# Optimization experiments

Hardware: AMD Instinct MI355X
Metric: run time of the kernel (lower is better)

## Reference

```python
import jax, jax.numpy as jnp
import numpy as np

B, S, H, NH, HD, L, I, M = 2, 2048, 768, 12, 64, 6, 3072, 256
VOCAB, TYPES = 30522, 2
EPS = 1e-6  # layernorm epsilon and FAVOR+ numerical stabilizer


def layer_norm(x, g, b):
    mu = jnp.mean(x, axis=-1, keepdims=True)
    var = jnp.mean(jax.lax.square(x), axis=-1, keepdims=True) - jax.lax.square(mu)
    return (x - mu) * jax.lax.rsqrt(var + EPS) * g + b


def favor_attention(q, k, v, mask, proj):
    # q,k,v: [B,S,NH,HD]; proj: [M,HD] random features; mask: [B,S] float
    dn = 1.0 / np.sqrt(np.sqrt(HD))      # data normalizer for softmax kernel
    ratio = 1.0 / np.sqrt(M)
    qn, kn = q * dn, k * dn
    qp = jnp.einsum('bsnd,md->bsnm', qn, proj)
    kp = jnp.einsum('bsnd,md->bsnm', kn, proj)
    qd = 0.5 * jnp.sum(qn * qn, axis=-1, keepdims=True)
    kd = 0.5 * jnp.sum(kn * kn, axis=-1, keepdims=True)
    # stabilizers: per-position max for queries, global (seq+feature) max for keys
    q_prime = ratio * (jnp.exp(qp - qd - jnp.max(qp, axis=-1, keepdims=True)) + EPS)
    k_prime = ratio * (jnp.exp(kp - kd - jnp.max(kp, axis=(1, 3), keepdims=True)) + EPS)
    k_prime = k_prime * mask[:, :, None, None]
    kv = jnp.einsum('bsnm,bsnd->bnmd', k_prime, v)          # [B,NH,M,HD]
    num = jnp.einsum('bsnm,bnmd->bsnd', q_prime, kv)        # [B,S,NH,HD]
    den = jnp.einsum('bsnm,bnm->bsn', q_prime, jnp.sum(k_prime, axis=1))
    return num / den[..., None]


def setup_inputs() -> dict:
    key = jax.random.key(0)
    ks = jax.random.split(key, 32)
    f = lambda i, shape, s=0.02: (jax.random.normal(ks[i], shape, jnp.float32) * s)
    inp = {
        'input_ids': jax.random.randint(ks[0], (B, S), 0, VOCAB, jnp.int32),
        'token_type_ids': jax.random.randint(ks[1], (B, S), 0, TYPES, jnp.int32),
        'position_ids': jnp.tile(jnp.arange(S, dtype=jnp.int32)[None, :], (B, 1)),
        'attention_mask': jnp.ones((B, S), jnp.int32),
        'word_emb': f(2, (VOCAB, H), 0.1),
        'pos_emb': f(3, (S, H), 0.1),
        'type_emb': f(4, (TYPES, H), 0.1),
        'emb_ln_g': jnp.ones((H,), jnp.float32),
        'emb_ln_b': jnp.zeros((H,), jnp.float32),
        'wq': f(5, (L, H, NH, HD)), 'bq': jnp.zeros((L, NH, HD), jnp.float32),
        'wk': f(6, (L, H, NH, HD)), 'bk': jnp.zeros((L, NH, HD), jnp.float32),
        'wv': f(7, (L, H, NH, HD)), 'bv': jnp.zeros((L, NH, HD), jnp.float32),
        'wo': f(8, (L, NH, HD, H)), 'bo': jnp.zeros((L, H), jnp.float32),
        'ln1_g': jnp.ones((L, H), jnp.float32), 'ln1_b': jnp.zeros((L, H), jnp.float32),
        'wi': f(9, (L, H, I)), 'bi': jnp.zeros((L, I), jnp.float32),
        'wo2': f(10, (L, I, H)), 'bo2': jnp.zeros((L, H), jnp.float32),
        'ln2_g': jnp.ones((L, H), jnp.float32), 'ln2_b': jnp.zeros((L, H), jnp.float32),
        'proj': jax.random.normal(ks[11], (L, M, HD), jnp.float32),
    }
    return inp


def reference(input_ids, token_type_ids, position_ids, attention_mask,
              word_emb, pos_emb, type_emb, emb_ln_g, emb_ln_b,
              wq, bq, wk, bk, wv, bv, wo, bo, ln1_g, ln1_b,
              wi, bi, wo2, bo2, ln2_g, ln2_b, proj):
    mask = attention_mask.astype(jnp.float32)
    x = word_emb[input_ids] + pos_emb[position_ids] + type_emb[token_type_ids]
    x = layer_norm(x, emb_ln_g, emb_ln_b)
    for l in range(L):
        q = jnp.einsum('bsh,hnd->bsnd', x, wq[l]) + bq[l]
        k = jnp.einsum('bsh,hnd->bsnd', x, wk[l]) + bk[l]
        v = jnp.einsum('bsh,hnd->bsnd', x, wv[l]) + bv[l]
        att = favor_attention(q, k, v, mask, proj[l])
        att = jnp.einsum('bsnd,ndh->bsh', att, wo[l]) + bo[l]
        a = layer_norm(att + x, ln1_g[l], ln1_b[l])
        inter = jax.nn.gelu(jnp.einsum('bsh,hi->bsi', a, wi[l]) + bi[l])
        out = jnp.einsum('bsi,ih->bsh', inter, wo2[l]) + bo2[l]
        x = layer_norm(out + a, ln2_g[l], ln2_b[l])
    return x
```

## Files before the change

### kernel.cpp

```cpp
#include <hip/hip_runtime.h>
#include <hip/hip_bf16.h>

#define B_ 2
#define S_ 2048
#define H_ 768
#define NH_ 12
#define HD_ 64
#define L_ 6
#define I_ 3072
#define M_ 256
#define BS_ 4096
#define R_ 49152
#define EPS_ 1e-6f
#define DN_ 0.35355339059327373f
#define RATIO_ 0.0625f

typedef __attribute__((ext_vector_type(8))) short bf16x8;
typedef __attribute__((ext_vector_type(4))) float f32x4;

__device__ __forceinline__ void gload16(const void* g, void* l) {
    __builtin_amdgcn_global_load_lds(
        (const __attribute__((address_space(1))) void*)g,
        (__attribute__((address_space(3))) void*)l, 16, 0, 0);
}

__device__ __forceinline__ float gelu_f(float x) {
    const float c = 0.7978845608028654f;
    float x3 = x * x * x;
    return 0.5f * x * (1.0f + tanhf(c * (x + 0.044715f * x3)));
}

__device__ __forceinline__ void blockReduceSum2(float& a, float& b) {
    __shared__ float sa[4], sb[4];
    int lane = threadIdx.x & 63, wid = threadIdx.x >> 6;
    #pragma unroll
    for (int off = 32; off; off >>= 1) {
        a += __shfl_down(a, off, 64);
        b += __shfl_down(b, off, 64);
    }
    __syncthreads();
    if (lane == 0) { sa[wid] = a; sb[wid] = b; }
    __syncthreads();
    a = sa[0] + sa[1] + sa[2] + sa[3];
    b = sb[0] + sb[1] + sb[2] + sb[3];
    __syncthreads();
}

__device__ __forceinline__ float blockReduceMax(float v) {
    __shared__ float sm[4];
    int lane = threadIdx.x & 63, wid = threadIdx.x >> 6;
    #pragma unroll
    for (int off = 32; off; off >>= 1) v = fmaxf(v, __shfl_down(v, off, 64));
    __syncthreads();
    if (lane == 0) sm[wid] = v;
    __syncthreads();
    float r = fmaxf(fmaxf(sm[0], sm[1]), fmaxf(sm[2], sm[3]));
    __syncthreads();
    return r;
}

__device__ __forceinline__ float blockReduceSum(float v) {
    __shared__ float sm[4];
    int lane = threadIdx.x & 63, wid = threadIdx.x >> 6;
    #pragma unroll
    for (int off = 32; off; off >>= 1) v += __shfl_down(v, off, 64);
    __syncthreads();
    if (lane == 0) sm[wid] = v;
    __syncthreads();
    float r = sm[0] + sm[1] + sm[2] + sm[3];
    __syncthreads();
    return r;
}

template<int ACT, int OUTMODE, int RMAXOUT>
__global__ __launch_bounds__(256) void gemm_mfma_kernel(
    const __hip_bfloat16* __restrict__ A, const __hip_bfloat16* __restrict__ BT,
    const float* __restrict__ bias, void* __restrict__ Cv,
    int N, int K, int lda, int ldb, int ldc, float alpha,
    float* __restrict__ rmaxp)
{
    __shared__ __align__(16) unsigned short As[2][128][32];
    __shared__ __align__(16) unsigned short Bs[2][128][32];
    __shared__ float rmx[128][2];
    const int tid = threadIdx.x, lane = tid & 63, wid = tid >> 6;
    const int wr = wid >> 1, wc = wid & 1;
    const size_t r0 = (size_t)blockIdx.y * 128;
    const int n0 = blockIdx.x * 128;

    const int srow = lane >> 2;
    const int selem = (lane & 3) * 8;
    const unsigned short* ga0 = (const unsigned short*)A + (r0 + wid * 32 + srow) * (size_t)lda + selem;
    const unsigned short* gb0 = (const unsigned short*)BT + ((size_t)n0 + wid * 32 + srow) * (size_t)ldb + selem;

    f32x4 acc[4][4];
    #pragma unroll
    for (int i = 0; i < 4; i++)
        #pragma unroll
        for (int j = 0; j < 4; j++)
            acc[i][j] = (f32x4){0.f, 0.f, 0.f, 0.f};

    gload16(ga0, &As[0][wid * 32][0]);
    gload16(ga0 + 16 * (size_t)lda, &As[0][wid * 32 + 16][0]);
    gload16(gb0, &Bs[0][wid * 32][0]);
    gload16(gb0 + 16 * (size_t)ldb, &Bs[0][wid * 32 + 16][0]);
    __syncthreads();

    int cur = 0;
    for (int k0 = 0; k0 < K; k0 += 32) {
        const int kn = k0 + 32;
        if (kn < K) {
            gload16(ga0 + kn, &As[cur ^ 1][wid * 32][0]);
            gload16(ga0 + kn + 16 * (size_t)lda, &As[cur ^ 1][wid * 32 + 16][0]);
            gload16(gb0 + kn, &Bs[cur ^ 1][wid * 32][0]);
            gload16(gb0 + kn + 16 * (size_t)ldb, &Bs[cur ^ 1][wid * 32 + 16][0]);
        }
        bf16x8 af[4], bfv[4];
        #pragma unroll
        for (int i = 0; i < 4; i++)
            af[i] = *(const bf16x8*)&As[cur][wr * 64 + i * 16 + (lane & 15)][(lane >> 4) * 8];
        #pragma unroll
        for (int j = 0; j < 4; j++)
            bfv[j] = *(const bf16x8*)&Bs[cur][wc * 64 + j * 16 + (lane & 15)][(lane >> 4) * 8];
        #pragma unroll
        for (int i = 0; i < 4; i++)
            #pragma unroll
            for (int j = 0; j < 4; j++)
                acc[i][j] = __builtin_amdgcn_mfma_f32_16x16x32_bf16(af[i], bfv[j], acc[i][j], 0, 0, 0);
        __syncthreads();
        cur ^= 1;
    }

    const int rr = (lane >> 4) * 4;
    const int cc = lane & 15;
    const size_t seg = (size_t)n0 / 768;
    const int colbase = n0 - (int)seg * 768;
    #pragma unroll
    for (int i = 0; i < 4; i++) {
        #pragma unroll
        for (int j = 0; j < 4; j++) {
            int colw = wc * 64 + j * 16 + cc;
            size_t col = (size_t)n0 + colw;
            float bv_ = bias ? bias[col] : 0.f;
            #pragma unroll
            for (int rg = 0; rg < 4; rg++) {
                size_t row = r0 + wr * 64 + i * 16 + rr + rg;
                float v = acc[i][j][rg] * alpha + bv_;
                if (ACT == 1) v = gelu_f(v);
                if (OUTMODE == 0)
                    ((float*)Cv)[row * ldc + col] = v;
                else if (OUTMODE == 1)
                    ((__hip_bfloat16*)Cv)[row * ldc + col] = __float2bfloat16(v);
                else
                    ((__hip_bfloat16*)Cv)[seg * ((size_t)BS_ * H_) + row * 768 + colbase + colw]
                        = __float2bfloat16(v);
            }
        }
    }
    if (RMAXOUT) {
        #pragma unroll
        for (int i = 0; i < 4; i++) {
            #pragma unroll
            for (int rg = 0; rg < 4; rg++) {
                float rm = -3.4e38f;
                #pragma unroll
                for (int j = 0; j < 4; j++) rm = fmaxf(rm, acc[i][j][rg] * alpha);
                #pragma unroll
                for (int off = 1; off <= 8; off <<= 1)
                    rm = fmaxf(rm, __shfl_xor(rm, off, 64));
                if ((lane & 15) == 0) rmx[wr * 64 + i * 16 + rr + rg][wc] = rm;
            }
        }
        __syncthreads();
        if (tid < 128)
            rmaxp[(size_t)blockIdx.x * R_ + r0 + tid] = fmaxf(rmx[tid][0], rmx[tid][1]);
    }
}

__global__ __launch_bounds__(256) void gemm_mfma_n64_kernel(
    const __hip_bfloat16* __restrict__ A, const __hip_bfloat16* __restrict__ BT,
    const float* __restrict__ bias, float* __restrict__ C,
    int K, int lda, int ldb, int ldc)
{
    __shared__ __align__(16) unsigned short As[2][128][32];
    __shared__ __align__(16) unsigned short Bs[2][64][32];
    const int tid = threadIdx.x, lane = tid & 63, wid = tid >> 6;
    const size_t r0 = (size_t)blockIdx.y * 128;
    const int n0 = blockIdx.x * 64;

    const int srow = lane >> 2, selem = (lane & 3) * 8;
    const unsigned short* ga0 = (const unsigned short*)A + (r0 + wid * 32 + srow) * (size_t)lda + selem;
    const unsigned short* gb0 = (const unsigned short*)BT + ((size_t)n0 + wid * 16 + srow) * (size_t)ldb + selem;

    f32x4 acc[2][4];
    #pragma unroll
    for (int i = 0; i < 2; i++)
        #pragma unroll
        for (int j = 0; j < 4; j++)
            acc[i][j] = (f32x4){0.f, 0.f, 0.f, 0.f};

    gload16(ga0, &As[0][wid * 32][0]);
    gload16(ga0 + 16 * (size_t)lda, &As[0][wid * 32 + 16][0]);
    gload16(gb0, &Bs[0][wid * 16][0]);
    __syncthreads();

    int cur = 0;
    for (int k0 = 0; k0 < K; k0 += 32) {
        const int kn = k0 + 32;
        if (kn < K) {
            gload16(ga0 + kn, &As[cur ^ 1][wid * 32][0]);
            gload16(ga0 + kn + 16 * (size_t)lda, &As[cur ^ 1][wid * 32 + 16][0]);
            gload16(gb0 + kn, &Bs[cur ^ 1][wid * 16][0]);
        }
        bf16x8 af[2], bfv[4];
        #pragma unroll
        for (int i = 0; i < 2; i++)
            af[i] = *(const bf16x8*)&As[cur][wid * 32 + i * 16 + (lane & 15)][(lane >> 4) * 8];
        #pragma unroll
        for (int j = 0; j < 4; j++)
            bfv[j] = *(const bf16x8*)&Bs[cur][j * 16 + (lane & 15)][(lane >> 4) * 8];
        #pragma unroll
        for (int i = 0; i < 2; i++)
            #pragma unroll
            for (int j = 0; j < 4; j++)
                acc[i][j] = __builtin_amdgcn_mfma_f32_16x16x32_bf16(af[i], bfv[j], acc[i][j], 0, 0, 0);
        __syncthreads();
        cur ^= 1;
    }

    const int rr = (lane >> 4) * 4, cc = lane & 15;
    #pragma unroll
    for (int i = 0; i < 2; i++) {
        #pragma unroll
        for (int j = 0; j < 4; j++) {
            int col = n0 + j * 16 + cc;
            float bv_ = bias ? bias[col] : 0.f;
            #pragma unroll
            for (int rg = 0; rg < 4; rg++) {
                size_t row = r0 + wid * 32 + i * 16 + rr + rg;
                C[row * (size_t)ldc + col] = acc[i][j][rg] + bv_;
            }
        }
    }
}

__global__ __launch_bounds__(256) void num_mfma_kernel(
    const __hip_bfloat16* __restrict__ QPb, const __hip_bfloat16* __restrict__ kvT,
    const float* __restrict__ den, __hip_bfloat16* __restrict__ ATT)
{
    __shared__ __align__(16) unsigned short As[2][128][32];
    __shared__ __align__(16) unsigned short Bs[2][64][32];
    const int tid = threadIdx.x, lane = tid & 63, wid = tid >> 6;
    const int s0 = blockIdx.x * 128;
    const int bn = blockIdx.y, b = bn / NH_, n = bn % NH_;

    const int srow = lane >> 2, selem = (lane & 3) * 8;
    const unsigned short* ga0 = (const unsigned short*)QPb + (size_t)b * S_ * (NH_ * M_) + n * M_
                              + ((size_t)s0 + wid * 32 + srow) * (NH_ * M_) + selem;
    const unsigned short* gb0 = (const unsigned short*)kvT + (size_t)bn * (HD_ * M_)
                              + ((size_t)wid * 16 + srow) * M_ + selem;

    f32x4 acc[2][4];
    #pragma unroll
    for (int i = 0; i < 2; i++)
        #pragma unroll
        for (int j = 0; j < 4; j++)
            acc[i][j] = (f32x4){0.f, 0.f, 0.f, 0.f};

    gload16(ga0, &As[0][wid * 32][0]);
    gload16(ga0 + 16 * (size_t)(NH_ * M_), &As[0][wid * 32 + 16][0]);
    gload16(gb0, &Bs[0][wid * 16][0]);
    __syncthreads();

    int cur = 0;
    for (int k0 = 0; k0 < M_; k0 += 32) {
        const int kn = k0 + 32;
        if (kn < M_) {
            gload16(ga0 + kn, &As[cur ^ 1][wid * 32][0]);
            gload16(ga0 + kn + 16 * (size_t)(NH_ * M_), &As[cur ^ 1][wid * 32 + 16][0]);
            gload16(gb0 + kn, &Bs[cur ^ 1][wid * 16][0]);
        }
        bf16x8 af[2], bfv[4];
        #pragma unroll
        for (int i = 0; i < 2; i++)
            af[i] = *(const bf16x8*)&As[cur][wid * 32 + i * 16 + (lane & 15)][(lane >> 4) * 8];
        #pragma unroll
        for (int j = 0; j < 4; j++)
            bfv[j] = *(const bf16x8*)&Bs[cur][j * 16 + (lane & 15)][(lane >> 4) * 8];
        #pragma unroll
        for (int i = 0; i < 2; i++)
            #pragma unroll
            for (int j = 0; j < 4; j++)
                acc[i][j] = __builtin_amdgcn_mfma_f32_16x16x32_bf16(af[i], bfv[j], acc[i][j], 0, 0, 0);
        __syncthreads();
        cur ^= 1;
    }

    const int rr = (lane >> 4) * 4, cc = lane & 15;
    #pragma unroll
    for (int i = 0; i < 2; i++) {
        #pragma unroll
        for (int rg = 0; rg < 4; rg++) {
            int s = s0 + wid * 32 + i * 16 + rr + rg;
            float inv = 1.0f / den[((size_t)b * S_ + s) * NH_ + n];
            #pragma unroll
            for (int j = 0; j < 4; j++)
                ATT[((size_t)b * S_ + s) * H_ + n * HD_ + j * 16 + cc]
                    = __float2bfloat16(acc[i][j][rg] * inv);
        }
    }
}

__global__ __launch_bounds__(256) void kv_splitk_kernel(
    const float* __restrict__ KP, const __hip_bfloat16* __restrict__ Vb, float* __restrict__ part)
{
    const int m0 = blockIdx.x * 64, bn = blockIdx.y, b = bn / NH_, n = bn % NH_;
    const int s0 = blockIdx.z * 256;
    __shared__ __align__(16) float As2[16][68];
    __shared__ __align__(16) float Bs2[16][68];
    const int tid = threadIdx.x, tx = tid & 15, ty = tid >> 4;
    float acc[4][4] = {};
    for (int ss = 0; ss < 256; ss += 16) {
        #pragma unroll
        for (int i = 0; i < 4; i++) {
            int idx = tid + i * 256;
            int kk = idx >> 6, c = idx & 63;
            size_t srow = (size_t)b * S_ + s0 + ss + kk;
            As2[kk][c] = KP[srow * (NH_ * M_) + n * M_ + m0 + c];
            Bs2[kk][c] = __bfloat162float(Vb[srow * H_ + n * HD_ + c]);
        }
        __syncthreads();
        #pragma unroll
        for (int kk = 0; kk < 16; kk++) {
            float4 av = *reinterpret_cast<const float4*>(&As2[kk][ty * 4]);
            float4 bv = *reinterpret_cast<const float4*>(&Bs2[kk][tx * 4]);
            float a4[4] = {av.x, av.y, av.z, av.w};
            float b4[4] = {bv.x, bv.y, bv.z, bv.w};
            #pragma unroll
            for (int i = 0; i < 4; i++)
                #pragma unroll
                for (int j = 0; j < 4; j++)
// ... 75 lines not shown
    const int* __restrict__ ids, const int* __restrict__ tts, const int* __restrict__ pos,
    const float* __restrict__ wemb, const float* __restrict__ pemb, const float* __restrict__ temb,
    const float* __restrict__ g, const float* __restrict__ bb,
    float* __restrict__ out, __hip_bfloat16* __restrict__ outb)
{
    size_t row = blockIdx.x;
    int id = ids[row], tt = tts[row], ps = pos[row];
    const float* w0 = wemb + (size_t)id * H_;
    const float* p0 = pemb + (size_t)ps * H_;
    const float* t0 = temb + (size_t)tt * H_;
    float vals[3], s1 = 0.f, s2 = 0.f;
    #pragma unroll
    for (int i = 0; i < 3; i++) {
        int h = threadIdx.x + i * 256;
        float v = w0[h] + p0[h] + t0[h];
        vals[i] = v; s1 += v; s2 += v * v;
    }
    blockReduceSum2(s1, s2);
    float mu = s1 * (1.0f / H_);
    float var = s2 * (1.0f / H_) - mu * mu;
    float rs = rsqrtf(var + EPS_);
    #pragma unroll
    for (int i = 0; i < 3; i++) {
        int h = threadIdx.x + i * 256;
        float y = (vals[i] - mu) * rs * g[h] + bb[h];
        out[row * H_ + h] = y;
        outb[row * H_ + h] = __float2bfloat16(y);
    }
}

__global__ __launch_bounds__(256) void add_ln_kernel(
    const float* __restrict__ P, const float* __restrict__ Q,
    const float* __restrict__ g, const float* __restrict__ bb,
    float* __restrict__ out, __hip_bfloat16* __restrict__ outb)
{
    size_t row = blockIdx.x;
    float vals[3], s1 = 0.f, s2 = 0.f;
    #pragma unroll
    for (int i = 0; i < 3; i++) {
        int h = threadIdx.x + i * 256;
        float v = P[row * H_ + h] + Q[row * H_ + h];
        vals[i] = v; s1 += v; s2 += v * v;
    }
    blockReduceSum2(s1, s2);
    float mu = s1 * (1.0f / H_);
    float var = s2 * (1.0f / H_) - mu * mu;
    float rs = rsqrtf(var + EPS_);
    #pragma unroll
    for (int i = 0; i < 3; i++) {
        int h = threadIdx.x + i * 256;
        float y = (vals[i] - mu) * rs * g[h] + bb[h];
        out[row * H_ + h] = y;
        if (outb) outb[row * H_ + h] = __float2bfloat16(y);
    }
}

__global__ __launch_bounds__(256) void rowsq_bf16_kernel(
    const __hip_bfloat16* __restrict__ X, float* __restrict__ out, float scale)
{
    int lane = threadIdx.x & 63, wid = threadIdx.x >> 6;
    size_t r = (size_t)blockIdx.x * 4 + wid;
    float v = __bfloat162float(X[r * 64 + lane]);
    float s = v * v;
    #pragma unroll
    for (int off = 32; off; off >>= 1) s += __shfl_down(s, off, 64);
    if (lane == 0) out[r] = scale * s;
}

__global__ __launch_bounds__(256) void gmax_kernel(
    const float* __restrict__ rmaxp, float* __restrict__ gmax)
{
    int bn = blockIdx.x, b = bn / NH_, n = bn % NH_;
    float mx = -3.4e38f;
    for (int s = threadIdx.x; s < S_; s += 256) {
        size_t r = ((size_t)b * S_ + s) * NH_ + n;
        mx = fmaxf(mx, fmaxf(rmaxp[r], rmaxp[R_ + r]));
    }
    mx = blockReduceMax(mx);
    if (threadIdx.x == 0) gmax[bn] = mx;
}

__global__ __launch_bounds__(256) void kprime_ksum_kernel(
    float* __restrict__ KP, const float* __restrict__ kd,
    const float* __restrict__ gmax, const int* __restrict__ amask,
    float* __restrict__ kpart)
{
    const int bn = blockIdx.x, chunk = blockIdx.y;
    const int b = bn / NH_, n = bn % NH_;
    const int m = threadIdx.x;
    const float gm = gmax[bn];
    float acc = 0.f;
    for (int si = 0; si < 64; si++) {
        size_t bs = (size_t)b * S_ + chunk * 64 + si;
        size_t r = bs * NH_ + n;
        float mk = (float)amask[bs];
        size_t e = r * M_ + m;
        float v = RATIO_ * (expf(KP[e] - kd[r] - gm) + EPS_) * mk;
        KP[e] = v;
        acc += v;
    }
    kpart[((size_t)bn * 32 + chunk) * M_ + m] = acc;
}

__global__ __launch_bounds__(256) void ksum_final_kernel(
    const float* __restrict__ part, float* __restrict__ ksum)
{
// ... 36 lines not shown
    const float* temb = (const float*)d_in[6];
    const float* elng = (const float*)d_in[7];
    const float* elnb = (const float*)d_in[8];
    const float* wq  = (const float*)d_in[9];
    const float* bq  = (const float*)d_in[10];
    const float* wk  = (const float*)d_in[11];
    const float* bk  = (const float*)d_in[12];
    const float* wv  = (const float*)d_in[13];
    const float* bv  = (const float*)d_in[14];
    const float* wo  = (const float*)d_in[15];
    const float* bo  = (const float*)d_in[16];
    const float* ln1g = (const float*)d_in[17];
    const float* ln1b = (const float*)d_in[18];
    const float* wi  = (const float*)d_in[19];
    const float* bi  = (const float*)d_in[20];
    const float* wo2 = (const float*)d_in[21];
    const float* bo2 = (const float*)d_in[22];
    const float* ln2g = (const float*)d_in[23];
    const float* ln2b = (const float*)d_in[24];
    const float* proj = (const float*)d_in[25];

    float* ws = (float*)d_ws;
    float* X    = ws;
    float* T2   = X + 3145728;
    float* BIG  = T2 + 3145728;
    float* U    = BIG + 12582912;
    __hip_bfloat16* Xb  = (__hip_bfloat16*)(U + 6291456);
    __hip_bfloat16* Qb  = (__hip_bfloat16*)((float*)Xb + 1572864);
    __hip_bfloat16* Kb  = Qb + 3145728;
    __hip_bfloat16* Vb  = Kb + 3145728;
    __hip_bfloat16* BF1 = Vb + 3145728;
    __hip_bfloat16* WT  = BF1 + 3145728;
    float* kvT_f = (float*)(WT + 7094272);
    __hip_bfloat16* kvT = (__hip_bfloat16*)kvT_f;
    float* KSUM  = kvT_f + 196608;
    float* KPART = KSUM + 6144;
    float* RMAXP = KPART + 196608;
    float* GMAX  = RMAXP + 98304;
    float* QD    = GMAX + 64;
    float* KD    = QD + 49152;
    float* DEN   = KD + 49152;
    float* BIASQ = DEN + 49152;
    float* T1    = (float*)d_out;

    __hip_bfloat16* wqT  = WT;
    __hip_bfloat16* wkT  = wqT + 589824;
    __hip_bfloat16* wvT  = wkT + 589824;
    __hip_bfloat16* woT  = wvT + 589824;
    __hip_bfloat16* wiT  = woT + 589824;
    __hip_bfloat16* wo2T = wiT + 2359296;
    __hip_bfloat16* projb = wo2T + 2359296;
    __hip_bfloat16* QPb = (__hip_bfloat16*)U;
    float* PART = U;
    __hip_bfloat16* BIGb = (__hip_bfloat16*)BIG;

    embed_ln_kernel<<<BS_, 256, 0, stream>>>(input_ids, token_type, position,
        wemb, pemb, temb, elng, elnb, X, Xb);

    const float sqscale = 0.5f * DN_ * DN_;
    for (int l = 0; l < L_; l++) {
        const float* wq_l = wq + (size_t)l * H_ * NH_ * HD_;
        const float* wk_l = wk + (size_t)l * H_ * NH_ * HD_;
        const float* wv_l = wv + (size_t)l * H_ * NH_ * HD_;
        const float* wo_l = wo + (size_t)l * NH_ * HD_ * H_;
        const float* bq_l = bq + (size_t)l * NH_ * HD_;
        const float* bk_l = bk + (size_t)l * NH_ * HD_;
        const float* bv_l = bv + (size_t)l * NH_ * HD_;
        const float* bo_l = bo + (size_t)l * H_;
        const float* wi_l = wi + (size_t)l * H_ * I_;
        const float* bi_l = bi + (size_t)l * I_;
        const float* wo2_l = wo2 + (size_t)l * I_ * H_;
        const float* bo2_l = bo2 + (size_t)l * H_;
        const float* proj_l = proj + (size_t)l * M_ * HD_;

        prep_kernel<<<6985, 256, 0, stream>>>(wq_l, wk_l, wv_l, wo_l, wi_l, wo2_l, proj_l,
            bq_l, bk_l, bv_l, wqT, wkT, wvT, woT, wiT, wo2T, projb, BIASQ);

        gemm_mfma_kernel<0,2,0><<<dim3(18,32), 256, 0, stream>>>(
            Xb, wqT, BIASQ, (void*)Qb, 2304, 768, 768, 768, 768, 1.f, nullptr);

        rowsq_bf16_kernel<<<2*R_/4, 256, 0, stream>>>(Qb, QD, sqscale);

        gemm_mfma_kernel<0,0,1><<<dim3(2,384), 256, 0, stream>>>(
            Kb, projb, nullptr, BIG, 256, 64, 64, 64, 256, DN_, RMAXP);
        gmax_kernel<<<B_*NH_, 256, 0, stream>>>(RMAXP, GMAX);
        kprime_ksum_kernel<<<dim3(B_*NH_, 32), 256, 0, stream>>>(BIG, KD, GMAX, amask, KPART);
        ksum_final_kernel<<<B_*NH_, 256, 0, stream>>>(KPART, KSUM);
        kv_splitk_kernel<<<dim3(4, B_*NH_, 8), 256, 0, stream>>>(BIG, Vb, PART);
        kvred_kernel<<<B_*NH_, 256, 0, stream>>>(PART, kvT);

        gemm_mfma_kernel<0,0,1><<<dim3(2,384), 256, 0, stream>>>(
            Qb, projb, nullptr, BIG, 256, 64, 64, 64, 256, DN_, RMAXP);
        qprime_den_kernel<<<R_, 256, 0, stream>>>(BIG, QD, KSUM, RMAXP, DEN, QPb);
        num_mfma_kernel<<<dim3(16, B_*NH_), 256, 0, stream>>>(QPb, kvT, DEN, BF1);

        gemm_mfma_n64_kernel<<<dim3(12,32), 256, 0, stream>>>(
            BF1, woT, bo_l, T1, 768, 768, 768, 768);
        add_ln_kernel<<<BS_, 256, 0, stream>>>(T1, X, ln1g + (size_t)l*H_, ln1b + (size_t)l*H_, T2, BF1);

        gemm_mfma_kernel<1,1,0><<<dim3(24,32), 256, 0, stream>>>(
            BF1, wiT, bi_l, (void*)BIGb, 3072, 768, 768, 768, 3072, 1.f, nullptr);
        gemm_mfma_n64_kernel<<<dim3(12,32), 256, 0, stream>>>(
            BIGb, wo2T, bo2_l, T1, 3072, 3072, 3072, 768);
        float* xout = (l == L_ - 1) ? (float*)d_out : X;
        add_ln_kernel<<<BS_, 256, 0, stream>>>(T1, T2, ln2g + (size_t)l*H_, ln2b + (size_t)l*H_, xout, Xb);
    }
}
```

Before: 1.918 ms.

## Add 256x128 GEMM tile, split-K FFN-out with fused reduce-LN, swizzle LDS

Introduces a larger 256x128 tile GEMM kernel for the QKV and FFN-in projections, and runs the FFN-out GEMM as 4-way split-K writing fp32 partials. A new add_ln4 kernel sums those partials with the bias and residual before the layer norm. An XOR swizzle is applied to the LDS layout in all MFMA GEMMs to reduce bank conflicts. The aim is more data reuse per block and more parallelism for the K=3072 GEMM, paid for with extra partial-sum memory traffic and higher register pressure.

Result: slower. 2.164 ms (+12.8%).

```diff
diff --git a/kernel.cpp b/kernel.cpp
--- a/kernel.cpp
+++ b/kernel.cpp
@@ -11,6 +11,7 @@
 #define M_ 256
 #define BS_ 4096
 #define R_ 49152
+#define NXH_ 3145728
 #define EPS_ 1e-6f
 #define DN_ 0.35355339059327373f
 #define RATIO_ 0.0625f
@@ -72,10 +73,109 @@
     return r;
 }
 
-template<int ACT, int OUTMODE, int RMAXOUT>
+
+template<int ACT, int OUTMODE>
+__global__ __launch_bounds__(256, 2) void gemm_big_kernel(
+    const __hip_bfloat16* __restrict__ A, const __hip_bfloat16* __restrict__ BT,
+    const float* __restrict__ bias, void* __restrict__ Cv,
+    int K, int lda, int ldb, int ldc,
+    float* __restrict__ p01, float* __restrict__ p23)
+{
+    __shared__ __align__(16) unsigned short As[2][256][32];
+    __shared__ __align__(16) unsigned short Bs[2][128][32];
+    const int tid = threadIdx.x, lane = tid & 63, wid = tid >> 6;
+    const int wrow = wid >> 1, wcol = wid & 1;
+    const size_t r0 = (size_t)blockIdx.y * 256;
+    const int n0 = blockIdx.x * 128;
+    const size_t kbase = (size_t)blockIdx.z * (size_t)K;
+
+    const int srow = lane >> 2;
+    const int selem = ((lane & 3) ^ ((srow >> 1) & 3)) * 8;
+    const unsigned short* gaw = (const unsigned short*)A + (r0 + wid * 64 + srow) * (size_t)lda + kbase + selem;
+    const unsigned short* gbw = (const unsigned short*)BT + ((size_t)n0 + wid * 32 + srow) * (size_t)ldb + kbase + selem;
+
+    f32x4 acc[8][4];
+    #pragma unroll
+    for (int i = 0; i < 8; i++)
+        #pragma unroll
+        for (int j = 0; j < 4; j++)
+            acc[i][j] = (f32x4){0.f, 0.f, 0.f, 0.f};
+
+    #pragma unroll
+    for (int c = 0; c < 4; c++)
+        gload16(gaw + (size_t)c * 16 * lda, &As[0][wid * 64 + c * 16][0]);
+    #pragma unroll
+    for (int c = 0; c < 2; c++)
+        gload16(gbw + (size_t)c * 16 * ldb, &Bs[0][wid * 32 + c * 16][0]);
+    __syncthreads();
+
+    const int lr = lane & 15;
+    const int rc8 = (((lane >> 4) ^ ((lr >> 1) & 3))) * 8;
+
+    int cur = 0;
+    for (int k0 = 0; k0 < K; k0 += 32) {
+        const int kn = k0 + 32;
+        if (kn < K) {
+            #pragma unroll
+            for (int c = 0; c < 4; c++)
+                gload16(gaw + (size_t)c * 16 * lda + kn, &As[cur ^ 1][wid * 64 + c * 16][0]);
+            #pragma unroll
+            for (int c = 0; c < 2; c++)
+                gload16(gbw + (size_t)c * 16 * ldb + kn, &Bs[cur ^ 1][wid * 32 + c * 16][0]);
+        }
+        bf16x8 af[8], bfv[4];
+        #pragma unroll
+        for (int i = 0; i < 8; i++)
+            af[i] = *(const bf16x8*)&As[cur][wrow * 128 + i * 16 + lr][rc8];
+        #pragma unroll
+        for (int j = 0; j < 4; j++)
+            bfv[j] = *(const bf16x8*)&Bs[cur][wcol * 64 + j * 16 + lr][rc8];
+        #pragma unroll
+        for (int i = 0; i < 8; i++)
+            #pragma unroll
+            for (int j = 0; j < 4; j++)
+                acc[i][j] = __builtin_amdgcn_mfma_f32_16x16x32_bf16(af[i], bfv[j], acc[i][j], 0, 0, 0);
+        __syncthreads();
+        cur ^= 1;
+    }
+
+    const int rr = (lane >> 4) * 4;
+    const int cc = lane & 15;
+    const size_t seg = (size_t)n0 / 768;
+    const int colbase = n0 - (int)seg * 768;
+    float* sdst = nullptr;
+    if (OUTMODE == 3)
+        sdst = (blockIdx.z < 2 ? p01 : p23) + (size_t)(blockIdx.z & 1) * NXH_;
+    #pragma unroll
+    for (int i = 0; i < 8; i++) {
+        #pragma unroll
+        for (int j = 0; j < 4; j++) {
+            int colw = wcol * 64 + j * 16 + cc;
+            size_t col = (size_t)n0 + colw;
+            float bv_ = (OUTMODE != 3 && bias) ? bias[col] : 0.f;
+            #pragma unroll
+            for (int rg = 0; rg < 4; rg++) {
+                size_t row = r0 + wrow * 128 + i * 16 + rr + rg;
+                float v = acc[i][j][rg] + bv_;
+                if (ACT == 1) v = gelu_f(v);
+                if (OUTMODE == 0)
+                    ((float*)Cv)[row * ldc + col] = v;
+                else if (OUTMODE == 1)
+                    ((__hip_bfloat16*)Cv)[row * ldc + col] = __float2bfloat16(v);
+                else if (OUTMODE == 2)
+                    ((__hip_bfloat16*)Cv)[seg * (size_t)NXH_ + row * 768 + colbase + colw]
+                        = __float2bfloat16(v);
+                else
+                    sdst[row * (size_t)ldc + col] = v;
+            }
+        }
+    }
+}
+
+template<int RMAXOUT>
 __global__ __launch_bounds__(256) void gemm_mfma_kernel(
     const __hip_bfloat16* __restrict__ A, const __hip_bfloat16* __restrict__ BT,
-    const float* __restrict__ bias, void* __restrict__ Cv,
+    void* __restrict__ Cv,
     int N, int K, int lda, int ldb, int ldc, float alpha,
     float* __restrict__ rmaxp)
 {
@@ -88,7 +188,7 @@
     const int n0 = blockIdx.x * 128;
 
     const int srow = lane >> 2;
-    const int selem = (lane & 3) * 8;
+    const int selem = ((lane & 3) ^ ((srow >> 1) & 3)) * 8;
     const unsigned short* ga0 = (const unsigned short*)A + (r0 + wid * 32 + srow) * (size_t)lda + selem;
     const unsigned short* gb0 = (const unsigned short*)BT + ((size_t)n0 + wid * 32 + srow) * (size_t)ldb + selem;
 
@@ -104,6 +204,9 @@
     gload16(gb0, &Bs[0][wid * 32][0]);
     gload16(gb0 + 16 * (size_t)ldb, &Bs[0][wid * 32 + 16][0]);
     __syncthreads();
+
+    const int lr = lane & 15;
+    const int rc8 = (((lane >> 4) ^ ((lr >> 1) & 3))) * 8;
 
     int cur = 0;
     for (int k0 = 0; k0 < K; k0 += 32) {
@@ -117,10 +220,10 @@
         bf16x8 af[4], bfv[4];
         #pragma unroll
         for (int i = 0; i < 4; i++)
-            af[i] = *(const bf16x8*)&As[cur][wr * 64 + i * 16 + (lane & 15)][(lane >> 4) * 8];
-        #pragma unroll
-        for (int j = 0; j < 4; j++)
-            bfv[j] = *(const bf16x8*)&Bs[cur][wc * 64 + j * 16 + (lane & 15)][(lane >> 4) * 8];
+            af[i] = *(const bf16x8*)&As[cur][wr * 64 + i * 16 + lr][rc8];
+        #pragma unroll
+        for (int j = 0; j < 4; j++)
+            bfv[j] = *(const bf16x8*)&Bs[cur][wc * 64 + j * 16 + lr][rc8];
         #pragma unroll
         for (int i = 0; i < 4; i++)
             #pragma unroll
@@ -132,27 +235,16 @@
 
     const int rr = (lane >> 4) * 4;
     const int cc = lane & 15;
-    const size_t seg = (size_t)n0 / 768;
-    const int colbase = n0 - (int)seg * 768;
     #pragma unroll
     for (int i = 0; i < 4; i++) {
         #pragma unroll
         for (int j = 0; j < 4; j++) {
             int colw = wc * 64 + j * 16 + cc;
             size_t col = (size_t)n0 + colw;
-            float bv_ = bias ? bias[col] : 0.f;
             #pragma unroll
             for (int rg = 0; rg < 4; rg++) {
                 size_t row = r0 + wr * 64 + i * 16 + rr + rg;
-                float v = acc[i][j][rg] * alpha + bv_;
-                if (ACT == 1) v = gelu_f(v);
-                if (OUTMODE == 0)
-                    ((float*)Cv)[row * ldc + col] = v;
-                else if (OUTMODE == 1)
-                    ((__hip_bfloat16*)Cv)[row * ldc + col] = __float2bfloat16(v);
-                else
-                    ((__hip_bfloat16*)Cv)[seg * ((size_t)BS_ * H_) + row * 768 + colbase + colw]
-                        = __float2bfloat16(v);
+                ((float*)Cv)[row * ldc + col] = acc[i][j][rg] * alpha;
             }
         }
     }
@@ -187,7 +279,8 @@
     const size_t r0 = (size_t)blockIdx.y * 128;
     const int n0 = blockIdx.x * 64;
 
-    const int srow = lane >> 2, selem = (lane & 3) * 8;
+    const int srow = lane >> 2;
+    const int selem = ((lane & 3) ^ ((srow >> 1) & 3)) * 8;
     const unsigned short* ga0 = (const unsigned short*)A + (r0 + wid * 32 + srow) * (size_t)lda + selem;
     const unsigned short* gb0 = (const unsigned short*)BT + ((size_t)n0 + wid * 16 + srow) * (size_t)ldb + selem;
 
@@ -202,6 +295,9 @@
     gload16(ga0 + 16 * (size_t)lda, &As[0][wid * 32 + 16][0]);
     gload16(gb0, &Bs[0][wid * 16][0]);
     __syncthreads();
+
+    const int lr = lane & 15;
+    const int rc8 = (((lane >> 4) ^ ((lr >> 1) & 3))) * 8;
 
     int cur = 0;
     for (int k0 = 0; k0 < K; k0 += 32) {
@@ -214,10 +310,10 @@
         bf16x8 af[2], bfv[4];
         #pragma unroll
         for (int i = 0; i < 2; i++)
-            af[i] = *(const bf16x8*)&As[cur][wid * 32 + i * 16 + (lane & 15)][(lane >> 4) * 8];
-        #pragma unroll
-        for (int j = 0; j < 4; j++)
-            bfv[j] = *(const bf16x8*)&Bs[cur][j * 16 + (lane & 15)][(lane >> 4) * 8];
+            af[i] = *(const bf16x8*)&As[cur][wid * 32 + i * 16 + lr][rc8];
+        #pragma unroll
+        for (int j = 0; j < 4; j++)
+            bfv[j] = *(const bf16x8*)&Bs[cur][j * 16 + lr][rc8];
         #pragma unroll
         for (int i = 0; i < 2; i++)
             #pragma unroll
@@ -253,7 +349,8 @@
     const int s0 = blockIdx.x * 128;
     const int bn = blockIdx.y, b = bn / NH_, n = bn % NH_;
 
-    const int srow = lane >> 2, selem = (lane & 3) * 8;
+    const int srow = lane >> 2;
+    const int selem = ((lane & 3) ^ ((srow >> 1) & 3)) * 8;
     const unsigned short* ga0 = (const unsigned short*)QPb + (size_t)b * S_ * (NH_ * M_) + n * M_
                               + ((size_t)s0 + wid * 32 + srow) * (NH_ * M_) + selem;
     const unsigned short* gb0 = (const unsigned short*)kvT + (size_t)bn * (HD_ * M_)
@@ -270,6 +367,9 @@
     gload16(ga0 + 16 * (size_t)(NH_ * M_), &As[0][wid * 32 + 16][0]);
     gload16(gb0, &Bs[0][wid * 16][0]);
     __syncthreads();
+
+    const int lr = lane & 15;
+    const int rc8 = (((lane >> 4) ^ ((lr >> 1) & 3))) * 8;
 
     int cur = 0;
     for (int k0 = 0; k0 < M_; k0 += 32) {
@@ -282,10 +382,10 @@
         bf16x8 af[2], bfv[4];
         #pragma unroll
         for (int i = 0; i < 2; i++)
-            af[i] = *(const bf16x8*)&As[cur][wid * 32 + i * 16 + (lane & 15)][(lane >> 4) * 8];
-        #pragma unroll
-        for (int j = 0; j < 4; j++)
-            bfv[j] = *(const bf16x8*)&Bs[cur][j * 16 + (lane & 15)][(lane >> 4) * 8];
+            af[i] = *(const bf16x8*)&As[cur][wid * 32 + i * 16 + lr][rc8];
+        #pragma unroll
+        for (int j = 0; j < 4; j++)
+            bfv[j] = *(const bf16x8*)&Bs[cur][j * 16 + lr][rc8];
         #pragma unroll
         for (int i = 0; i < 2; i++)
             #pragma unroll
@@ -467,6 +567,34 @@
         float y = (vals[i] - mu) * rs * g[h] + bb[h];
         out[row * H_ + h] = y;
         if (outb) outb[row * H_ + h] = __float2bfloat16(y);
+    }
+}
+
+__global__ __launch_bounds__(256) void add_ln4_kernel(
+    const float* __restrict__ p01, const float* __restrict__ p23,
+    const float* __restrict__ bias, const float* __restrict__ Q,
+    const float* __restrict__ g, const float* __restrict__ bb,
+    float* __restrict__ out, __hip_bfloat16* __restrict__ outb)
+{
+    size_t row = blockIdx.x;
+    float vals[3], s1 = 0.f, s2 = 0.f;
+    #pragma unroll
+    for (int i = 0; i < 3; i++) {
+        int h = threadIdx.x + i * 256;
+        size_t e = row * H_ + h;
+        float v = p01[e] + p01[NXH_ + e] + p23[e] + p23[NXH_ + e] + bias[h] + Q[e];
+        vals[i] = v; s1 += v; s2 += v * v;
+    }
+    blockReduceSum2(s1, s2);
+    float mu = s1 * (1.0f / H_);
+    float var = s2 * (1.0f / H_) - mu * mu;
+    float rs = rsqrtf(var + EPS_);
+    #pragma unroll
+    for (int i = 0; i < 3; i++) {
+        int h = threadIdx.x + i * 256;
+        float y = (vals[i] - mu) * rs * g[h] + bb[h];
+        out[row * H_ + h] = y;
+        outb[row * H_ + h] = __float2bfloat16(y);
     }
 }
 
@@ -609,6 +737,8 @@
     __hip_bfloat16* projb = wo2T + 2359296;
     __hip_bfloat16* QPb = (__hip_bfloat16*)U;
     float* PART = U;
+    float* P01  = BIG + 6291456;
+    float* P23  = U;
     __hip_bfloat16* BIGb = (__hip_bfloat16*)BIG;
 
     embed_ln_kernel<<<BS_, 256, 0, stream>>>(input_ids, token_type, position,
@@ -633,21 +763,21 @@
         prep_kernel<<<6985, 256, 0, stream>>>(wq_l, wk_l, wv_l, wo_l, wi_l, wo2_l, proj_l,
             bq_l, bk_l, bv_l, wqT, wkT, wvT, woT, wiT, wo2T, projb, BIASQ);
 
-        gemm_mfma_kernel<0,2,0><<<dim3(18,32), 256, 0, stream>>>(
-            Xb, wqT, BIASQ, (void*)Qb, 2304, 768, 768, 768, 768, 1.f, nullptr);
+        gemm_big_kernel<0,2><<<dim3(18,16), 256, 0, stream>>>(
+            Xb, wqT, BIASQ, (void*)Qb, 768, 768, 768, 768, nullptr, nullptr);
 
         rowsq_bf16_kernel<<<2*R_/4, 256, 0, stream>>>(Qb, QD, sqscale);
 
-        gemm_mfma_kernel<0,0,1><<<dim3(2,384), 256, 0, stream>>>(
-            Kb, projb, nullptr, BIG, 256, 64, 64, 64, 256, DN_, RMAXP);
+        gemm_mfma_kernel<1><<<dim3(2,384), 256, 0, stream>>>(
+            Kb, projb, BIG, 256, 64, 64, 64, 256, DN_, RMAXP);
         gmax_kernel<<<B_*NH_, 256, 0, stream>>>(RMAXP, GMAX);
         kprime_ksum_kernel<<<dim3(B_*NH_, 32), 256, 0, stream>>>(BIG, KD, GMAX, amask, KPART);
         ksum_final_kernel<<<B_*NH_, 256, 0, stream>>>(KPART, KSUM);
         kv_splitk_kernel<<<dim3(4, B_*NH_, 8), 256, 0, stream>>>(BIG, Vb, PART);
         kvred_kernel<<<B_*NH_, 256, 0, stream>>>(PART, kvT);
 
-        gemm_mfma_kernel<0,0,1><<<dim3(2,384), 256, 0, stream>>>(
-            Qb, projb, nullptr, BIG, 256, 64, 64, 64, 256, DN_, RMAXP);
+        gemm_mfma_kernel<1><<<dim3(2,384), 256, 0, stream>>>(
+            Qb, projb, BIG, 256, 64, 64, 64, 256, DN_, RMAXP);
         qprime_den_kernel<<<R_, 256, 0, stream>>>(BIG, QD, KSUM, RMAXP, DEN, QPb);
         num_mfma_kernel<<<dim3(16, B_*NH_), 256, 0, stream>>>(QPb, kvT, DEN, BF1);
 
@@ -655,11 +785,13 @@
             BF1, woT, bo_l, T1, 768, 768, 768, 768);
         add_ln_kernel<<<BS_, 256, 0, stream>>>(T1, X, ln1g + (size_t)l*H_, ln1b + (size_t)l*H_, T2, BF1);
 
-        gemm_mfma_kernel<1,1,0><<<dim3(24,32), 256, 0, stream>>>(
-            BF1, wiT, bi_l, (void*)BIGb, 3072, 768, 768, 768, 3072, 1.f, nullptr);
-        gemm_mfma_n64_kernel<<<dim3(12,32), 256, 0, stream>>>(
-            BIGb, wo2T, bo2_l, T1, 3072, 3072, 3072, 768);
+        gemm_big_kernel<1,1><<<dim3(24,16), 256, 0, stream>>>(
+            BF1, wiT, bi_l, (void*)BIGb, 768, 768, 768, 3072, nullptr, nullptr);
+
+        gemm_big_kernel<0,3><<<dim3(6,16,4), 256, 0, stream>>>(
+            BIGb, wo2T, nullptr, nullptr, 768, 3072, 3072, 768, P01, P23);
         float* xout = (l == L_ - 1) ? (float*)d_out : X;
-        add_ln_kernel<<<BS_, 256, 0, stream>>>(T1, T2, ln2g + (size_t)l*H_, ln2b + (size_t)l*H_, xout, Xb);
-    }
-}
+        add_ln4_kernel<<<BS_, 256, 0, stream>>>(P01, P23, bo2_l, T2,
+            ln2g + (size_t)l*H_, ln2b + (size_t)l*H_, xout, Xb);
+    }
+}
```

## Add triple-buffered GEMM pipeline with LDS XOR swizzle and MFMA priority

Applied to the files above, without the earlier changes.

Adds new GEMM kernels for the QKV, FFN-in, attention-out and FFN-out projections. They keep three LDS stages with explicit vmcnt waits and raw barriers, so global-to-LDS loads run two tiles ahead of compute, and they raise wave priority around the MFMA block. The existing GEMM and the num kernel get an XOR swizzle on LDS columns to cut bank conflicts on fragment reads. The cost is more shared memory per block, which may lower occupancy, and hand-tuned waitcnt counts that depend on exact load counts.

Result: no change. 1.898 ms (-1.1%).

```diff
diff --git a/kernel.cpp b/kernel.cpp
--- a/kernel.cpp
+++ b/kernel.cpp
@@ -11,6 +11,7 @@
 #define M_ 256
 #define BS_ 4096
 #define R_ 49152
+#define NXH_ 3145728
 #define EPS_ 1e-6f
 #define DN_ 0.35355339059327373f
 #define RATIO_ 0.0625f
@@ -72,10 +73,173 @@
     return r;
 }
 
-template<int ACT, int OUTMODE, int RMAXOUT>
+template<int ACT, int OUTMODE>
+__global__ __launch_bounds__(256) void gemm_pipe3_kernel(
+    const __hip_bfloat16* __restrict__ A, const __hip_bfloat16* __restrict__ BT,
+    const float* __restrict__ bias, void* __restrict__ Cv,
+    int K, int lda, int ldb, int ldc)
+{
+    __shared__ __align__(16) unsigned short As[3][128][32];
+    __shared__ __align__(16) unsigned short Bs[3][128][32];
+    const int tid = threadIdx.x, lane = tid & 63, wid = tid >> 6;
+    const int wr = wid >> 1, wc = wid & 1;
+    const size_t r0 = (size_t)blockIdx.y * 128;
+    const int n0 = blockIdx.x * 128;
+
+    const int srow = lane >> 2;
+    const int selem = ((lane & 3) ^ ((srow >> 1) & 3)) * 8;
+    const unsigned short* ga0 = (const unsigned short*)A + (r0 + wid * 32 + srow) * (size_t)lda + selem;
+    const unsigned short* gb0 = (const unsigned short*)BT + ((size_t)n0 + wid * 32 + srow) * (size_t)ldb + selem;
+
+    f32x4 acc[4][4];
+    #pragma unroll
+    for (int i = 0; i < 4; i++)
+        #pragma unroll
+        for (int j = 0; j < 4; j++)
+            acc[i][j] = (f32x4){0.f, 0.f, 0.f, 0.f};
+
+    const int lr = lane & 15;
+    const int rc8 = (((lane >> 4) ^ ((lr >> 1) & 3))) * 8;
+
+#define STAGE_(t) { const int bb_ = (t) % 3; const int kk_ = (t) * 32;            \
+    gload16(ga0 + kk_, &As[bb_][wid * 32][0]);                                    \
+    gload16(ga0 + kk_ + 16 * (size_t)lda, &As[bb_][wid * 32 + 16][0]);            \
+    gload16(gb0 + kk_, &Bs[bb_][wid * 32][0]);                                    \
+    gload16(gb0 + kk_ + 16 * (size_t)ldb, &Bs[bb_][wid * 32 + 16][0]); }
+
+#define ITER_(t, VMSTR, DOSTAGE) {                                                \
+    if (DOSTAGE) STAGE_((t) + 2);                                                 \
+    asm volatile("s_waitcnt vmcnt(" VMSTR ")" ::: "memory");                      \
+    __builtin_amdgcn_sched_barrier(0);                                            \
+    __builtin_amdgcn_s_barrier();                                                 \
+    __builtin_amdgcn_sched_barrier(0);                                            \
+    const int bb_ = (t) % 3;                                                      \
+    bf16x8 af[4], bfv[4];                                                         \
+    _Pragma("unroll") for (int i = 0; i < 4; i++)                                 \
+        af[i] = *(const bf16x8*)&As[bb_][wr * 64 + i * 16 + lr][rc8];             \
+    _Pragma("unroll") for (int j = 0; j < 4; j++)                                 \
+        bfv[j] = *(const bf16x8*)&Bs[bb_][wc * 64 + j * 16 + lr][rc8];            \
+    __builtin_amdgcn_s_setprio(1);                                                \
+    _Pragma("unroll") for (int i = 0; i < 4; i++)                                 \
+        _Pragma("unroll") for (int j = 0; j < 4; j++)                             \
+            acc[i][j] = __builtin_amdgcn_mfma_f32_16x16x32_bf16(af[i], bfv[j], acc[i][j], 0, 0, 0); \
+    __builtin_amdgcn_s_setprio(0);                                                \
+    __builtin_amdgcn_s_barrier();                                                 \
+    __builtin_amdgcn_sched_barrier(0); }
+
+    const int nT = K >> 5;
+    STAGE_(0); STAGE_(1);
+    for (int t = 0; t < nT - 2; ++t) ITER_(t, "8", true);
+    ITER_(nT - 2, "4", false);
+    ITER_(nT - 1, "0", false);
+#undef ITER_
+#undef STAGE_
+
+    const int rr = (lane >> 4) * 4;
+    const int cc = lane & 15;
+    const size_t seg = (size_t)n0 / 768;
+    const int colbase = n0 - (int)seg * 768;
+    #pragma unroll
+    for (int i = 0; i < 4; i++) {
+        #pragma unroll
+        for (int j = 0; j < 4; j++) {
+            int colw = wc * 64 + j * 16 + cc;
+            size_t col = (size_t)n0 + colw;
+            float bv_ = bias ? bias[col] : 0.f;
+            #pragma unroll
+            for (int rg = 0; rg < 4; rg++) {
+                size_t row = r0 + wr * 64 + i * 16 + rr + rg;
+                float v = acc[i][j][rg] + bv_;
+                if (ACT == 1) v = gelu_f(v);
+                if (OUTMODE == 1)
+                    ((__hip_bfloat16*)Cv)[row * (size_t)ldc + col] = __float2bfloat16(v);
+                else
+                    ((__hip_bfloat16*)Cv)[seg * (size_t)NXH_ + row * 768 + colbase + colw]
+                        = __float2bfloat16(v);
+            }
+        }
+    }
+}
+
+__global__ __launch_bounds__(256) void gemm_pipe3_n64_kernel(
+    const __hip_bfloat16* __restrict__ A, const __hip_bfloat16* __restrict__ BT,
+    const float* __restrict__ bias, float* __restrict__ C,
+    int K, int lda, int ldb, int ldc)
+{
+    __shared__ __align__(16) unsigned short As[3][128][32];
+    __shared__ __align__(16) unsigned short Bs[3][64][32];
+    const int tid = threadIdx.x, lane = tid & 63, wid = tid >> 6;
+    const size_t r0 = (size_t)blockIdx.y * 128;
+    const int n0 = blockIdx.x * 64;
+
+    const int srow = lane >> 2;
+    const int selem = ((lane & 3) ^ ((srow >> 1) & 3)) * 8;
+    const unsigned short* ga0 = (const unsigned short*)A + (r0 + wid * 32 + srow) * (size_t)lda + selem;
+    const unsigned short* gb0 = (const unsigned short*)BT + ((size_t)n0 + wid * 16 + srow) * (size_t)ldb + selem;
+
+    f32x4 acc[2][4];
+    #pragma unroll
+    for (int i = 0; i < 2; i++)
+        #pragma unroll
+        for (int j = 0; j < 4; j++)
+            acc[i][j] = (f32x4){0.f, 0.f, 0.f, 0.f};
+
+    const int lr = lane & 15;
+    const int rc8 = (((lane >> 4) ^ ((lr >> 1) & 3))) * 8;
+
+#define STAGE_(t) { const int bb_ = (t) % 3; const int kk_ = (t) * 32;            \
+    gload16(ga0 + kk_, &As[bb_][wid * 32][0]);                                    \
+    gload16(ga0 + kk_ + 16 * (size_t)lda, &As[bb_][wid * 32 + 16][0]);            \
+    gload16(gb0 + kk_, &Bs[bb_][wid * 16][0]); }
+
+#define ITER_(t, VMSTR, DOSTAGE) {                                                \
+    if (DOSTAGE) STAGE_((t) + 2);                                                 \
+    asm volatile("s_waitcnt vmcnt(" VMSTR ")" ::: "memory");                      \
+    __builtin_amdgcn_sched_barrier(0);                                            \
+    __builtin_amdgcn_s_barrier();                                                 \
+    __builtin_amdgcn_sched_barrier(0);                                            \
+    const int bb_ = (t) % 3;                                                      \
+    bf16x8 af[2], bfv[4];                                                         \
+    _Pragma("unroll") for (int i = 0; i < 2; i++)                                 \
+        af[i] = *(const bf16x8*)&As[bb_][wid * 32 + i * 16 + lr][rc8];            \
+    _Pragma("unroll") for (int j = 0; j < 4; j++)                                 \
+        bfv[j] = *(const bf16x8*)&Bs[bb_][j * 16 + lr][rc8];                      \
+    __builtin_amdgcn_s_setprio(1);                                                \
+    _Pragma("unroll") for (int i = 0; i < 2; i++)                                 \
+        _Pragma("unroll") for (int j = 0; j < 4; j++)                             \
+            acc[i][j] = __builtin_amdgcn_mfma_f32_16x16x32_bf16(af[i], bfv[j], acc[i][j], 0, 0, 0); \
+    __builtin_amdgcn_s_setprio(0);                                                \
+    __builtin_amdgcn_s_barrier();                                                 \
+    __builtin_amdgcn_sched_barrier(0); }
+
+    const int nT = K >> 5;
+    STAGE_(0); STAGE_(1);
+    for (int t = 0; t < nT - 2; ++t) ITER_(t, "6", true);
+    ITER_(nT - 2, "3", false);
+    ITER_(nT - 1, "0", false);
+#undef ITER_
+#undef STAGE_
+
+    const int rr = (lane >> 4) * 4, cc = lane & 15;
+    #pragma unroll
+    for (int i = 0; i < 2; i++) {
+        #pragma unroll
+        for (int j = 0; j < 4; j++) {
+            int col = n0 + j * 16 + cc;
+            float bv_ = bias ? bias[col] : 0.f;
+            #pragma unroll
+            for (int rg = 0; rg < 4; rg++) {
+                size_t row = r0 + wid * 32 + i * 16 + rr + rg;
+                C[row * (size_t)ldc + col] = acc[i][j][rg] + bv_;
+            }
+        }
+    }
+}
+
+template<int RMAXOUT>
 __global__ __launch_bounds__(256) void gemm_mfma_kernel(
     const __hip_bfloat16* __restrict__ A, const __hip_bfloat16* __restrict__ BT,
-    const float* __restrict__ bias, void* __restrict__ Cv,
+    void* __restrict__ Cv,
     int N, int K, int lda, int ldb, int ldc, float alpha,
     float* __restrict__ rmaxp)
 {
@@ -88,7 +252,7 @@
     const int n0 = blockIdx.x * 128;
 
     const int srow = lane >> 2;
-    const int selem = (lane & 3) * 8;
+    const int selem = ((lane & 3) ^ ((srow >> 1) & 3)) * 8;
     const unsigned short* ga0 = (const unsigned short*)A + (r0 + wid * 32 + srow) * (size_t)lda + selem;
     const unsigned short* gb0 = (const unsigned short*)BT + ((size_t)n0 + wid * 32 + srow) * (size_t)ldb + selem;
 
@@ -104,6 +268,9 @@
     gload16(gb0, &Bs[0][wid * 32][0]);
     gload16(gb0 + 16 * (size_t)ldb, &Bs[0][wid * 32 + 16][0]);
     __syncthreads();
+
+    const int lr = lane & 15;
+    const int rc8 = (((lane >> 4) ^ ((lr >> 1) & 3))) * 8;
 
     int cur = 0;
     for (int k0 = 0; k0 < K; k0 += 32) {
@@ -117,10 +284,10 @@
         bf16x8 af[4], bfv[4];
         #pragma unroll
         for (int i = 0; i < 4; i++)
-            af[i] = *(const bf16x8*)&As[cur][wr * 64 + i * 16 + (lane & 15)][(lane >> 4) * 8];
+            af[i] = *(const bf16x8*)&As[cur][wr * 64 + i * 16 + lr][rc8];
         #pragma unroll
         for (int j = 0; j < 4; j++)
-            bfv[j] = *(const bf16x8*)&Bs[cur][wc * 64 + j * 16 + (lane & 15)][(lane >> 4) * 8];
+            bfv[j] = *(const bf16x8*)&Bs[cur][wc * 64 + j * 16 + lr][rc8];
         #pragma unroll
         for (int i = 0; i < 4; i++)
             #pragma unroll
@@ -132,27 +299,16 @@
 
     const int rr = (lane >> 4) * 4;
     const int cc = lane & 15;
-    const size_t seg = (size_t)n0 / 768;
-    const int colbase = n0 - (int)seg * 768;
     #pragma unroll
     for (int i = 0; i < 4; i++) {
         #pragma unroll
         for (int j = 0; j < 4; j++) {
             int colw = wc * 64 + j * 16 + cc;
             size_t col = (size_t)n0 + colw;
-            float bv_ = bias ? bias[col] : 0.f;
             #pragma unroll
             for (int rg = 0; rg < 4; rg++) {
                 size_t row = r0 + wr * 64 + i * 16 + rr + rg;
-                float v = acc[i][j][rg] * alpha + bv_;
-                if (ACT == 1) v = gelu_f(v);
-                if (OUTMODE == 0)
-                    ((float*)Cv)[row * ldc + col] = v;
-                else if (OUTMODE == 1)
-                    ((__hip_bfloat16*)Cv)[row * ldc + col] = __float2bfloat16(v);
-                else
-                    ((__hip_bfloat16*)Cv)[seg * ((size_t)BS_ * H_) + row * 768 + colbase + colw]
-                        = __float2bfloat16(v);
+                ((float*)Cv)[row * ldc + col] = acc[i][j][rg] * alpha;
             }
         }
     }
@@ -176,73 +332,6 @@
     }
 }
 
-__global__ __launch_bounds__(256) void gemm_mfma_n64_kernel(
-    const __hip_bfloat16* __restrict__ A, const __hip_bfloat16* __restrict__ BT,
-    const float* __restrict__ bias, float* __restrict__ C,
-    int K, int lda, int ldb, int ldc)
-{
-    __shared__ __align__(16) unsigned short As[2][128][32];
-    __shared__ __align__(16) unsigned short Bs[2][64][32];
-    const int tid = threadIdx.x, lane = tid & 63, wid = tid >> 6;
-    const size_t r0 = (size_t)blockIdx.y * 128;
-    const int n0 = blockIdx.x * 64;
-
-    const int srow = lane >> 2, selem = (lane & 3) * 8;
-    const unsigned short* ga0 = (const unsigned short*)A + (r0 + wid * 32 + srow) * (size_t)lda + selem;
-    const unsigned short* gb0 = (const unsigned short*)BT + ((size_t)n0 + wid * 16 + srow) * (size_t)ldb + selem;
-
-    f32x4 acc[2][4];
-    #pragma unroll
-    for (int i = 0; i < 2; i++)
-        #pragma unroll
-        for (int j = 0; j < 4; j++)
-            acc[i][j] = (f32x4){0.f, 0.f, 0.f, 0.f};
-
-    gload16(ga0, &As[0][wid * 32][0]);
-    gload16(ga0 + 16 * (size_t)lda, &As[0][wid * 32 + 16][0]);
-    gload16(gb0, &Bs[0][wid * 16][0]);
-    __syncthreads();
-
-    int cur = 0;
-    for (int k0 = 0; k0 < K; k0 += 32) {
-        const int kn = k0 + 32;
-        if (kn < K) {
-            gload16(ga0 + kn, &As[cur ^ 1][wid * 32][0]);
-            gload16(ga0 + kn + 16 * (size_t)lda, &As[cur ^ 1][wid * 32 + 16][0]);
-            gload16(gb0 + kn, &Bs[cur ^ 1][wid * 16][0]);
-        }
-        bf16x8 af[2], bfv[4];
-        #pragma unroll
-        for (int i = 0; i < 2; i++)
-            af[i] = *(const bf16x8*)&As[cur][wid * 32 + i * 16 + (lane & 15)][(lane >> 4) * 8];
-        #pragma unroll
-        for (int j = 0; j < 4; j++)
-            bfv[j] = *(const bf16x8*)&Bs[cur][j * 16 + (lane & 15)][(lane >> 4) * 8];
-        #pragma unroll
-        for (int i = 0; i < 2; i++)
-            #pragma unroll
-            for (int j = 0; j < 4; j++)
-                acc[i][j] = __builtin_amdgcn_mfma_f32_16x16x32_bf16(af[i], bfv[j], acc[i][j], 0, 0, 0);
-        __syncthreads();
-        cur ^= 1;
-    }
-
-    const int rr = (lane >> 4) * 4, cc = lane & 15;
-    #pragma unroll
-    for (int i = 0; i < 2; i++) {
-        #pragma unroll
-        for (int j = 0; j < 4; j++) {
-            int col = n0 + j * 16 + cc;
-            float bv_ = bias ? bias[col] : 0.f;
-            #pragma unroll
-            for (int rg = 0; rg < 4; rg++) {
-                size_t row = r0 + wid * 32 + i * 16 + rr + rg;
-                C[row * (size_t)ldc + col] = acc[i][j][rg] + bv_;
-            }
-        }
-    }
-}
-
 __global__ __launch_bounds__(256) void num_mfma_kernel(
     const __hip_bfloat16* __restrict__ QPb, const __hip_bfloat16* __restrict__ kvT,
     const float* __restrict__ den, __hip_bfloat16* __restrict__ ATT)
@@ -253,7 +342,8 @@
     const int s0 = blockIdx.x * 128;
     const int bn = blockIdx.y, b = bn / NH_, n = bn % NH_;
 
-    const int srow = lane >> 2, selem = (lane & 3) * 8;
+    const int srow = lane >> 2;
+    const int selem = ((lane & 3) ^ ((srow >> 1) & 3)) * 8;
     const unsigned short* ga0 = (const unsigned short*)QPb + (size_t)b * S_ * (NH_ * M_) + n * M_
                               + ((size_t)s0 + wid * 32 + srow) * (NH_ * M_) + selem;
     const unsigned short* gb0 = (const unsigned short*)kvT + (size_t)bn * (HD_ * M_)
@@ -270,6 +360,9 @@
     gload16(ga0 + 16 * (size_t)(NH_ * M_), &As[0][wid * 32 + 16][0]);
     gload16(gb0, &Bs[0][wid * 16][0]);
     __syncthreads();
+
+    const int lr = lane & 15;
+    const int rc8 = (((lane >> 4) ^ ((lr >> 1) & 3))) * 8;
 
     int cur = 0;
     for (int k0 = 0; k0 < M_; k0 += 32) {
@@ -282,10 +375,10 @@
         bf16x8 af[2], bfv[4];
         #pragma unroll
         for (int i = 0; i < 2; i++)
-            af[i] = *(const bf16x8*)&As[cur][wid * 32 + i * 16 + (lane & 15)][(lane >> 4) * 8];
+            af[i] = *(const bf16x8*)&As[cur][wid * 32 + i * 16 + lr][rc8];
         #pragma unroll
         for (int j = 0; j < 4; j++)
-            bfv[j] = *(const bf16x8*)&Bs[cur][j * 16 + (lane & 15)][(lane >> 4) * 8];
+            bfv[j] = *(const bf16x8*)&Bs[cur][j * 16 + lr][rc8];
         #pragma unroll
         for (int i = 0; i < 2; i++)
             #pragma unroll
@@ -633,31 +726,32 @@
         prep_kernel<<<6985, 256, 0, stream>>>(wq_l, wk_l, wv_l, wo_l, wi_l, wo2_l, proj_l,
             bq_l, bk_l, bv_l, wqT, wkT, wvT, woT, wiT, wo2T, projb, BIASQ);
 
-        gemm_mfma_kernel<0,2,0><<<dim3(18,32), 256, 0, stream>>>(
-            Xb, wqT, BIASQ, (void*)Qb, 2304, 768, 768, 768, 768, 1.f, nullptr);
+        gemm_pipe3_kernel<0,2><<<dim3(18,32), 256, 0, stream>>>(
+            Xb, wqT, BIASQ, (void*)Qb, 768, 768, 768, 768);
 
         rowsq_bf16_kernel<<<2*R_/4, 256, 0, stream>>>(Qb, QD, sqscale);
 
-        gemm_mfma_kernel<0,0,1><<<dim3(2,384), 256, 0, stream>>>(
-            Kb, projb, nullptr, BIG, 256, 64, 64, 64, 256, DN_, RMAXP);
+        gemm_mfma_kernel<1><<<dim3(2,384), 256, 0, stream>>>(
+            Kb, projb, BIG, 256, 64, 64, 64, 256, DN_, RMAXP);
         gmax_kernel<<<B_*NH_, 256, 0, stream>>>(RMAXP, GMAX);
         kprime_ksum_kernel<<<dim3(B_*NH_, 32), 256, 0, stream>>>(BIG, KD, GMAX, amask, KPART);
         ksum_final_kernel<<<B_*NH_, 256, 0, stream>>>(KPART, KSUM);
         kv_splitk_kernel<<<dim3(4, B_*NH_, 8), 256, 0, stream>>>(BIG, Vb, PART);
         kvred_kernel<<<B_*NH_, 256, 0, stream>>>(PART, kvT);
 
-        gemm_mfma_kernel<0,0,1><<<dim3(2,384), 256, 0, stream>>>(
-            Qb, projb, nullptr, BIG, 256, 64, 64, 64, 256, DN_, RMAXP);
+        gemm_mfma_kernel<1><<<dim3(2,384), 256, 0, stream>>>(
+            Qb, projb, BIG, 256, 64, 64, 64, 256, DN_, RMAXP);
         qprime_den_kernel<<<R_, 256, 0, stream>>>(BIG, QD, KSUM, RMAXP, DEN, QPb);
         num_mfma_kernel<<<dim3(16, B_*NH_), 256, 0, stream>>>(QPb, kvT, DEN, BF1);
 
-        gemm_mfma_n64_kernel<<<dim3(12,32), 256, 0, stream>>>(
+        gemm_pipe3_n64_kernel<<<dim3(12,32), 256, 0, stream>>>(
             BF1, woT, bo_l, T1, 768, 768, 768, 768);
         add_ln_kernel<<<BS_, 256, 0, stream>>>(T1, X, ln1g + (size_t)l*H_, ln1b + (size_t)l*H_, T2, BF1);
 
-        gemm_mfma_kernel<1,1,0><<<dim3(24,32), 256, 0, stream>>>(
-            BF1, wiT, bi_l, (void*)BIGb, 3072, 768, 768, 768, 3072, 1.f, nullptr);
-        gemm_mfma_n64_kernel<<<dim3(12,32), 256, 0, stream>>>(
+        gemm_pipe3_kernel<1,1><<<dim3(24,32), 256, 0, stream>>>(
+            BF1, wiT, bi_l, (void*)BIGb, 768, 768, 768, 3072);
+
+        gemm_pipe3_n64_kernel<<<dim3(12,32), 256, 0, stream>>>(
             BIGb, wo2T, bo2_l, T1, 3072, 3072, 3072, 768);
         float* xout = (l == L_ - 1) ? (float*)d_out : X;
         add_ln_kernel<<<BS_, 256, 0, stream>>>(T1, T2, ln2g + (size_t)l*H_, ln2b + (size_t)l*H_, xout, Xb);
```
